# Optimization experiments

Measured on AMD Instinct MI355X. Metric: run time of the kernel, lower is better.

## Reference

```python
import jax, jax.numpy as jnp
import numpy as np

B, T, D_IN, D_OUT, H = 4, 2048, 1024, 1024, 16
HD = D_OUT // H

def setup_inputs() -> dict:
    key = jax.random.key(0)
    ks = jax.random.split(key, 9)
    s_in = 1.0 / np.sqrt(D_IN)
    s_out = 1.0 / np.sqrt(D_OUT)
    return {
        "x": jax.random.normal(ks[0], (B, T, D_IN), jnp.float32),
        "w_q": jax.random.uniform(ks[1], (D_IN, D_OUT), jnp.float32, -s_in, s_in),
        "b_q": jax.random.uniform(ks[2], (D_OUT,), jnp.float32, -s_in, s_in),
        "w_k": jax.random.uniform(ks[3], (D_IN, D_OUT), jnp.float32, -s_in, s_in),
        "b_k": jax.random.uniform(ks[4], (D_OUT,), jnp.float32, -s_in, s_in),
        "w_v": jax.random.uniform(ks[5], (D_IN, D_OUT), jnp.float32, -s_in, s_in),
        "b_v": jax.random.uniform(ks[6], (D_OUT,), jnp.float32, -s_in, s_in),
        "w_o": jax.random.uniform(ks[7], (D_OUT, D_OUT), jnp.float32, -s_out, s_out),
        "b_o": jax.random.uniform(ks[8], (D_OUT,), jnp.float32, -s_out, s_out),
    }

def reference(x, w_q, b_q, w_k, b_k, w_v, b_v, w_o, b_o):
    b, t, _ = x.shape
    # projections -> [b, h, t, hd]
    def split_heads(y):
        return y.reshape(b, t, H, HD).transpose(0, 2, 1, 3)
    q = split_heads(x @ w_q + b_q)
    k = split_heads(x @ w_k + b_k)
    v = split_heads(x @ w_v + b_v)
    scores = jnp.einsum('bhqd,bhkd->bhqk', q, k)
    causal = jnp.triu(jnp.ones((t, t), dtype=bool), k=1)
    scores = jnp.where(causal, -jnp.inf, scores)
    weights = jax.nn.softmax(scores / np.sqrt(HD), axis=-1)
    # dropout_rate = 0.0 -> identity
    ctx = jnp.einsum('bhqk,bhkd->bhqd', weights, v)
    ctx = ctx.transpose(0, 2, 1, 3).reshape(b, t, D_OUT)
    return ctx @ w_o + b_o
```

## Files before the change

### kernel.cpp

```cpp
#include <hip/hip_runtime.h>
#include <hip/hip_bf16.h>
#include <stdint.h>

#define B_N 4
#define T_N 2048
#define D_N 1024
#define H_N 16
#define HD_N 64

typedef __bf16 bf16x8 __attribute__((ext_vector_type(8)));
typedef unsigned short u16x8 __attribute__((ext_vector_type(8)));
typedef unsigned short u16x4 __attribute__((ext_vector_type(4)));
typedef float f32x4 __attribute__((ext_vector_type(4)));
typedef float f32x16 __attribute__((ext_vector_type(16)));

static __device__ __forceinline__ unsigned short f2bf(float f) {
    union { float f; unsigned u; } v; v.f = f;
    unsigned r = v.u + 0x7fffu + ((v.u >> 16) & 1u);
    return (unsigned short)(r >> 16);
}
static __device__ __forceinline__ float bf2f(unsigned short s) {
    union { unsigned u; float f; } v; v.u = ((unsigned)s) << 16;
    return v.f;
}
static __device__ __forceinline__ bf16x8 as_bf(u16x8 v) {
    return __builtin_bit_cast(bf16x8, v);
}
static __device__ __forceinline__ unsigned packbf(float a, float b) {
    union { float f; unsigned u; } x, y; x.f = a; y.f = b;
    return (x.u >> 16) | (y.u & 0xffff0000u);
}
static __device__ __forceinline__ void gload_lds16(const void* g, void* l) {
    __builtin_amdgcn_global_load_lds(
        (const __attribute__((address_space(1))) void*)g,
        (__attribute__((address_space(3))) void*)l, 16, 0, 0);
}

__global__ __launch_bounds__(256) void cvt_x_kernel(const float* __restrict__ x,
                                                    unsigned short* __restrict__ xb) {
    int i = (blockIdx.x * 256 + threadIdx.x) * 8;
    f32x4 a = *(const f32x4*)(x + i);
    f32x4 b = *(const f32x4*)(x + i + 4);
    u16x8 o;
    o[0] = f2bf(a[0]); o[1] = f2bf(a[1]); o[2] = f2bf(a[2]); o[3] = f2bf(a[3]);
    o[4] = f2bf(b[0]); o[5] = f2bf(b[1]); o[6] = f2bf(b[2]); o[7] = f2bf(b[3]);
    *(u16x8*)(xb + i) = o;
}

__global__ __launch_bounds__(256) void cvt_w_t_kernel(
        const float* __restrict__ w0, const float* __restrict__ w1,
        const float* __restrict__ w2, const float* __restrict__ w3,
        unsigned short* __restrict__ o0, unsigned short* __restrict__ o1,
        unsigned short* __restrict__ o2, unsigned short* __restrict__ o3) {
    __shared__ float tile[32][33];
    const float* w; unsigned short* o;
    switch (blockIdx.z) {
        case 0:  w = w0; o = o0; break;
        case 1:  w = w1; o = o1; break;
        case 2:  w = w2; o = o2; break;
        default: w = w3; o = o3; break;
    }
    int n0 = blockIdx.x * 32, k0 = blockIdx.y * 32;
    int tx = threadIdx.x & 31, ty = threadIdx.x >> 5;
    #pragma unroll
    for (int r = 0; r < 4; ++r)
        tile[ty + r * 8][tx] = w[(k0 + ty + r * 8) * 1024 + n0 + tx];
    __syncthreads();
    #pragma unroll
    for (int r = 0; r < 4; ++r)
        o[(n0 + ty + r * 8) * 1024 + k0 + tx] = f2bf(tile[tx][ty + r * 8]);
}

#define BM 128
#define BN 128
#define BK 64

__global__ __launch_bounds__(256) void qkv_gemm_kernel(
        const unsigned short* __restrict__ xb,
        const unsigned short* __restrict__ wt,
        const float* __restrict__ bq, const float* __restrict__ bk,
        const float* __restrict__ bv,
        unsigned short* __restrict__ qws, unsigned short* __restrict__ kws,
        unsigned short* __restrict__ vtws) {
    __shared__ unsigned short As[BM * BK];
    __shared__ unsigned short Bs[BN * BK];
    const int tid = threadIdx.x;
    const int lane = tid & 63, wid = tid >> 6;
    const int wr = wid >> 1, wc = wid & 1;
    const int l15 = lane & 15, lg = lane >> 4;
    const int mbase = blockIdx.y * BM;
    const int nbase = blockIdx.x * BN;

    const int rsub = lane >> 3;
    const int gsw  = (lane & 7) ^ rsub;
    const unsigned short* asrc0 = xb + (mbase + wid * 32 + rsub) * 1024 + gsw * 8;
    const unsigned short* bsrc0 = wt + (nbase + wid * 32 + rsub) * 1024 + gsw * 8;
    char* adst0 = (char*)As + wid * 4096;
    char* bdst0 = (char*)Bs + wid * 4096;

    f32x4 acc[4][4] = {};

    for (int k0 = 0; k0 < 1024; k0 += BK) {
        __syncthreads();
        #pragma unroll
        for (int i = 0; i < 4; ++i)
            gload_lds16(asrc0 + i * 8 * 1024 + k0, adst0 + i * 1024);
        #pragma unroll
        for (int i = 0; i < 4; ++i)
            gload_lds16(bsrc0 + i * 8 * 1024 + k0, bdst0 + i * 1024);
        __syncthreads();
        #pragma unroll
        for (int kk = 0; kk < 2; ++kk) {
            bf16x8 a[4], b[4];
            #pragma unroll
            for (int mi = 0; mi < 4; ++mi) {
                int m = wr * 64 + mi * 16 + l15;
                int g = (kk * 4 + lg) ^ (m & 7);
                a[mi] = as_bf(*(const u16x8*)(As + m * 64 + (g << 3)));
            }
            #pragma unroll
            for (int ni = 0; ni < 4; ++ni) {
                int n = wc * 64 + ni * 16 + l15;
                int g = (kk * 4 + lg) ^ (n & 7);
                b[ni] = as_bf(*(const u16x8*)(Bs + n * 64 + (g << 3)));
            }
            #pragma unroll
            for (int mi = 0; mi < 4; ++mi)
                #pragma unroll
                for (int ni = 0; ni < 4; ++ni)
                    acc[mi][ni] = __builtin_amdgcn_mfma_f32_16x16x32_bf16(
                        a[mi], b[ni], acc[mi][ni], 0, 0, 0);
        }
    }

    const int mat = nbase >> 10;
    const float* bias = (mat == 0) ? bq : (mat == 1) ? bk : bv;
    #pragma unroll
    for (int ni = 0; ni < 4; ++ni) {
        int cg = (nbase & 1023) + wc * 64 + ni * 16 + l15;
        float bb = bias[cg];
        int h = cg >> 6, hd = cg & 63;
        #pragma unroll
        for (int mi = 0; mi < 4; ++mi) {
            int row = mbase + wr * 64 + mi * 16 + lg * 4;
            int bidx = row >> 11;
            int t = row & 2047;
            if (mat == 2) {
                u16x4 pv;
                #pragma unroll
                for (int r = 0; r < 4; ++r) pv[r] = f2bf(acc[mi][ni][r] + bb);
                *(u16x4*)(vtws + ((bidx * 16 + h) * 64 + hd) * 2048 + t) = pv;
            } else {
                unsigned short* dst =
                    ((mat == 0) ? qws : kws) + ((bidx * 16 + h) * 2048 + t) * 64 + hd;
                #pragma unroll
                for (int r = 0; r < 4; ++r) dst[r * 64] = f2bf(acc[mi][ni][r] + bb);
            }
        }
    }
}

#define AQB 128
#define AKV 64

__global__ __launch_bounds__(256, 3) void attn_kernel(
        const unsigned short* __restrict__ qws,
        const unsigned short* __restrict__ kws,
        const unsigned short* __restrict__ vtws,
        unsigned short* __restrict__ ctx) {
    __shared__ unsigned short Ks[2][AKV * 64];
    __shared__ unsigned short Vs[2][64 * AKV];
    __shared__ unsigned short Os[4][32 * 64];

    const int tid = threadIdx.x;
    const int lane = tid & 63, wid = tid >> 6;
    const int l31 = lane & 31, hi = lane >> 5;
    const int qb = 15 - (int)(blockIdx.x >> 6);
    const int bh = blockIdx.x & 63;
    const int qbase = qb * AQB;
    const int qwbase = qbase + wid * 32;
    const unsigned short* qp = qws + bh * 2048 * 64;
    const unsigned short* kp = kws + bh * 2048 * 64;
    const unsigned short* vp = vtws + bh * 64 * 2048;

    const float QSCALE = 0.125f * 1.44269504f;
    bf16x8 qf[4];
    #pragma unroll
    for (int ks = 0; ks < 4; ++ks) {
        u16x8 v = *(const u16x8*)(qp + (qwbase + l31) * 64 + ks * 16 + hi * 8);
        u16x8 o;
        #pragma unroll
        for (int e = 0; e < 8; ++e) o[e] = f2bf(bf2f(v[e]) * QSCALE);
        qf[ks] = as_bf(o);
    }

    f32x16 acc0 = {}, acc1 = {};
    float m_run = -1e30f, lsum = 0.f;

    const int nt = 2 * qb + 2;
    const int wnt = 2 * qb + 1 + (wid >> 1);

    u16x8 kr[2], vr[2];
    #pragma unroll
    for (int it = 0; it < 2; ++it) {
        int flat = it * 256 + tid, r = flat >> 3, g = flat & 7;
        kr[it] = *(const u16x8*)(kp + r * 64 + g * 8);
        vr[it] = *(const u16x8*)(vp + r * 2048 + g * 8);
    }
    #pragma unroll
    for (int it = 0; it < 2; ++it) {
        int flat = it * 256 + tid, r = flat >> 3, g = flat & 7;
        *(u16x8*)(&Ks[0][r * 64 + ((g ^ (r & 7)) << 3)]) = kr[it];
        *(u16x8*)(&Vs[0][r * 64 + ((g ^ (r & 7)) << 3)]) = vr[it];
    }
    __syncthreads();

    for (int t = 0; t < nt; ++t) {
        const int cur = t & 1;
        const int kt = t * AKV;
        if (t + 1 < nt) {
            int kt2 = kt + AKV;
            #pragma unroll
            for (int it = 0; it < 2; ++it) {
                int flat = it * 256 + tid, r = flat >> 3, g = flat & 7;
                kr[it] = *(const u16x8*)(kp + (kt2 + r) * 64 + g * 8);
                vr[it] = *(const u16x8*)(vp + r * 2048 + kt2 + g * 8);
            }
        }
        if (t < wnt) {
            const unsigned short* kb = &Ks[cur][0];
            const unsigned short* vb = &Vs[cur][0];
            #pragma unroll
            for (int half = 0; half < 2; ++half) {
                const int kvbase = kt + half * 32;
                if (kvbase > qwbase + 31) continue;
                f32x16 st = {};
                #pragma unroll
                for (int ks = 0; ks < 4; ++ks) {
                    int row = half * 32 + l31;
                    int g = (ks * 2 + hi) ^ (row & 7);
                    bf16x8 kf = as_bf(*(const u16x8*)(kb + row * 64 + (g << 3)));
                    st = __builtin_amdgcn_mfma_f32_32x32x16_bf16(kf, qf[ks], st, 0, 0, 0);
                }
                if (kvbase + 31 > qwbase) {
                    int q = qwbase + l31;
                    #pragma unroll
                    for (int r = 0; r < 16; ++r) {
                        int kv = kvbase + (r & 3) + 8 * (r >> 2) + 4 * hi;
                        if (kv > q) st[r] = -1e30f;
                    }
                }
                float pmax = st[0];
                #pragma unroll
                for (int r = 1; r < 16; ++r) pmax = fmaxf(pmax, st[r]);
                pmax = fmaxf(pmax, __shfl_xor(pmax, 32));
                if (!__all(pmax - m_run <= 11.5f)) {
                    float mnew = fmaxf(m_run, pmax);
                    float alpha = __builtin_amdgcn_exp2f(m_run - mnew);
                    m_run = mnew;
                    lsum *= alpha;
                    #pragma unroll
                    for (int r = 0; r < 16; ++r) { acc0[r] *= alpha; acc1[r] *= alpha; }
                }
                float p[16];
                float ls = 0.f;
                #pragma unroll
                for (int r = 0; r < 16; ++r) {
                    p[r] = __builtin_amdgcn_exp2f(st[r] - m_run);
                    ls += p[r];
                }
                lsum += ls;
                unsigned c[8], x[8];
                #pragma unroll
                for (int i = 0; i < 8; ++i) c[i] = packbf(p[2 * i], p[2 * i + 1]);
                #pragma unroll
                for (int i = 0; i < 8; ++i) x[i] = (unsigned)__shfl_xor((int)c[i], 32);
                union { u16x8 v; unsigned w[4]; } pb0, pb1;
                pb0.w[0] = hi ? x[2] : c[0];
                pb0.w[1] = hi ? x[3] : c[1];
                pb0.w[2] = hi ? c[2] : x[0];
                pb0.w[3] = hi ? c[3] : x[1];
                pb1.w[0] = hi ? x[6] : c[4];
                pb1.w[1] = hi ? x[7] : c[5];
                pb1.w[2] = hi ? c[6] : x[4];
                pb1.w[3] = hi ? c[7] : x[5];
                #pragma unroll
                for (int db = 0; db < 2; ++db) {
                    f32x16& accd = db ? acc1 : acc0;
                    #pragma unroll
                    for (int ks2 = 0; ks2 < 2; ++ks2) {
                        int row = db * 32 + l31;
                        int g = (half * 4 + ks2 * 2 + hi) ^ (row & 7);
                        bf16x8 vf = as_bf(*(const u16x8*)(vb + row * 64 + (g << 3)));
                        accd = __builtin_amdgcn_mfma_f32_32x32x16_bf16(
                            vf, ks2 ? pb1.v : pb0.v, accd, 0, 0, 0);
                    }
                }
            }
        }
        __syncthreads();
        if (t + 1 < nt) {
            unsigned short* dk = &Ks[cur ^ 1][0];
            unsigned short* dv = &Vs[cur ^ 1][0];
            #pragma unroll
            for (int it = 0; it < 2; ++it) {
                int flat = it * 256 + tid, r = flat >> 3, g = flat & 7;
                *(u16x8*)(dk + r * 64 + ((g ^ (r & 7)) << 3)) = kr[it];
                *(u16x8*)(dv + r * 64 + ((g ^ (r & 7)) << 3)) = vr[it];
            }
        }
        __syncthreads();
    }

    lsum += __shfl_xor(lsum, 32);
    float rinv = __builtin_amdgcn_rcpf(lsum);
    unsigned short* ow = &Os[wid][0];
    #pragma unroll
    for (int db = 0; db < 2; ++db) {
        const f32x16& accd = db ? acc1 : acc0;
        #pragma unroll
        for (int r = 0; r < 16; r += 2) {
            int d = db * 32 + (r & 3) + 8 * (r >> 2) + 4 * hi;
            unsigned w = packbf(accd[r] * rinv, accd[r + 1] * rinv);
            int g = (d >> 3) ^ (l31 & 7);
            *(unsigned*)(ow + l31 * 64 + (g << 3) + (d & 7)) = w;
        }
    }
    __syncthreads();
    const int bidx = bh >> 4, h = bh & 15;
    #pragma unroll
    for (int rr = 0; rr < 4; ++rr) {
        int flat = rr * 64 + lane;
        int q = flat >> 3, g = flat & 7;
        u16x8 v = *(const u16x8*)(ow + q * 64 + ((g ^ (q & 7)) << 3));
        int qg = qbase + wid * 32 + q;
        *(u16x8*)(ctx + (bidx * 2048 + qg) * 1024 + h * 64 + g * 8) = v;
    }
}

__global__ __launch_bounds__(256) void out_gemm_kernel(
        const unsigned short* __restrict__ ctx,
        const unsigned short* __restrict__ wot,
        const float* __restrict__ bo,
        float* __restrict__ out) {
    __shared__ unsigned short As[BM * BK];
    __shared__ unsigned short Bs[BN * BK];
    const int tid = threadIdx.x;
    const int lane = tid & 63, wid = tid >> 6;
    const int wr = wid >> 1, wc = wid & 1;
    const int l15 = lane & 15, lg = lane >> 4;
    const int mbase = blockIdx.y * BM;
    const int nbase = blockIdx.x * BN;

    const int rsub = lane >> 3;
    const int gsw  = (lane & 7) ^ rsub;
    const unsigned short* asrc0 = ctx + (mbase + wid * 32 + rsub) * 1024 + gsw * 8;
    const unsigned short* bsrc0 = wot + (nbase + wid * 32 + rsub) * 1024 + gsw * 8;
    char* adst0 = (char*)As + wid * 4096;
    char* bdst0 = (char*)Bs + wid * 4096;

    f32x4 acc[4][4] = {};

    for (int k0 = 0; k0 < 1024; k0 += BK) {
        __syncthreads();
        #pragma unroll
        for (int i = 0; i < 4; ++i)
            gload_lds16(asrc0 + i * 8 * 1024 + k0, adst0 + i * 1024);
        #pragma unroll
        for (int i = 0; i < 4; ++i)
            gload_lds16(bsrc0 + i * 8 * 1024 + k0, bdst0 + i * 1024);
        __syncthreads();
        #pragma unroll
        for (int kk = 0; kk < 2; ++kk) {
            bf16x8 a[4], b[4];
            #pragma unroll
            for (int mi = 0; mi < 4; ++mi) {
                int m = wr * 64 + mi * 16 + l15;
                int g = (kk * 4 + lg) ^ (m & 7);
                a[mi] = as_bf(*(const u16x8*)(As + m * 64 + (g << 3)));
            }
            #pragma unroll
            for (int ni = 0; ni < 4; ++ni) {
                int n = wc * 64 + ni * 16 + l15;
                int g = (kk * 4 + lg) ^ (n & 7);
                b[ni] = as_bf(*(const u16x8*)(Bs + n * 64 + (g << 3)));
            }
            #pragma unroll
            for (int mi = 0; mi < 4; ++mi)
                #pragma unroll
                for (int ni = 0; ni < 4; ++ni)
                    acc[mi][ni] = __builtin_amdgcn_mfma_f32_16x16x32_bf16(
                        a[mi], b[ni], acc[mi][ni], 0, 0, 0);
        }
    }

    #pragma unroll
    for (int ni = 0; ni < 4; ++ni) {
        int ncol = nbase + wc * 64 + ni * 16 + l15;
        float bb = bo[ncol];
        #pragma unroll
        for (int mi = 0; mi < 4; ++mi) {
            int row = mbase + wr * 64 + mi * 16 + lg * 4;
            #pragma unroll
            for (int r = 0; r < 4; ++r)
                out[(row + r) * 1024 + ncol] = acc[mi][ni][r] + bb;
        }
    }
}

extern "C" void kernel_launch(void* const* d_in, const int* in_sizes, int n_in,
                              void* d_out, int out_size, void* d_ws, size_t ws_size,
                              hipStream_t stream) {
    const float* x  = (const float*)d_in[0];
    const float* wq = (const float*)d_in[1];
    const float* bq = (const float*)d_in[2];
    const float* wk = (const float*)d_in[3];
    const float* bk = (const float*)d_in[4];
    const float* wv = (const float*)d_in[5];
    const float* bv = (const float*)d_in[6];
    const float* wo = (const float*)d_in[7];
    const float* bo = (const float*)d_in[8];
    float* out = (float*)d_out;

    char* ws = (char*)d_ws;
    unsigned short* xb   = (unsigned short*)(ws);
    unsigned short* wqt  = (unsigned short*)(ws + (16u << 20));
    unsigned short* wkt  = (unsigned short*)(ws + (18u << 20));
    unsigned short* wvt  = (unsigned short*)(ws + (20u << 20));
    unsigned short* wot  = (unsigned short*)(ws + (22u << 20));
    unsigned short* qws  = (unsigned short*)(ws + (24u << 20));
    unsigned short* kws  = (unsigned short*)(ws + (40u << 20));
    unsigned short* vtws = (unsigned short*)(ws + (56u << 20));
    unsigned short* ctx  = (unsigned short*)(ws + (72u << 20));

    cvt_x_kernel<<<4096, 256, 0, stream>>>(x, xb);
    cvt_w_t_kernel<<<dim3(32, 32, 4), 256, 0, stream>>>(wq, wk, wv, wo,
                                                        wqt, wkt, wvt, wot);
    qkv_gemm_kernel<<<dim3(24, 64), 256, 0, stream>>>(xb, wqt, bq, bk, bv,
                                                      qws, kws, vtws);
    attn_kernel<<<1024, 256, 0, stream>>>(qws, kws, vtws, ctx);
    out_gemm_kernel<<<dim3(8, 64), 256, 0, stream>>>(ctx, wot, bo, out);
}
```

Measured before the change: 250.1 us.

## Double-buffer LDS in projection GEMMs and remap blocks across XCDs

Both projection GEMMs now keep two LDS buffers and prefetch the k-tile two steps ahead with direct global-to-LDS loads. Explicit vmcnt waits, barriers and setprio around the MFMA bursts let memory traffic overlap with compute instead of stalling on a full sync every k-step. The launch becomes a 1D grid whose block index is remapped so that consecutive tiles land on the same XCD, which should improve L2 reuse of shared A and B panels. This doubles LDS use per block, which may lower occupancy, and the hand-written waitcnt counts must match the number of loads in flight.

```diff
diff --git a/kernel.cpp b/kernel.cpp
--- a/kernel.cpp
+++ b/kernel.cpp
@@ -71,9 +71,7 @@
         o[(n0 + ty + r * 8) * 1024 + k0 + tx] = f2bf(tile[tx][ty + r * 8]);
 }
 
-#define BM 128
-#define BN 128
-#define BK 64
+#define GNT 16
 
 __global__ __launch_bounds__(256) void qkv_gemm_kernel(
         const unsigned short* __restrict__ xb,
@@ -82,54 +80,101 @@
         const float* __restrict__ bv,
         unsigned short* __restrict__ qws, unsigned short* __restrict__ kws,
         unsigned short* __restrict__ vtws) {
-    __shared__ unsigned short As[BM * BK];
-    __shared__ unsigned short Bs[BN * BK];
+    __shared__ unsigned short As[2][128 * 64];
+    __shared__ unsigned short Bs[2][128 * 64];
     const int tid = threadIdx.x;
     const int lane = tid & 63, wid = tid >> 6;
     const int wr = wid >> 1, wc = wid & 1;
     const int l15 = lane & 15, lg = lane >> 4;
-    const int mbase = blockIdx.y * BM;
-    const int nbase = blockIdx.x * BN;
-
+    const int cpx = (int)gridDim.x >> 3;
+    const int s = ((int)blockIdx.x & 7) * cpx + ((int)blockIdx.x >> 3);
+    const int by = s / 24, bx = s - by * 24;
+    const int mbase = by * 128, nbase = bx * 128;
     const int rsub = lane >> 3;
     const int gsw  = (lane & 7) ^ rsub;
-    const unsigned short* asrc0 = xb + (mbase + wid * 32 + rsub) * 1024 + gsw * 8;
-    const unsigned short* bsrc0 = wt + (nbase + wid * 32 + rsub) * 1024 + gsw * 8;
-    char* adst0 = (char*)As + wid * 4096;
-    char* bdst0 = (char*)Bs + wid * 4096;
+    const unsigned short* ags = xb + (mbase + wid * 8 + rsub) * 1024 + gsw * 8;
+    const unsigned short* bgs = wt + (nbase + wid * 8 + rsub) * 1024 + gsw * 8;
+    const int dstE = wid * 8 * 64;
 
     f32x4 acc[4][4] = {};
 
-    for (int k0 = 0; k0 < 1024; k0 += BK) {
-        __syncthreads();
+    auto STAGE = [&](int T, int BUF) {
+        const unsigned short* a_ = ags + T * 64;
+        const unsigned short* b_ = bgs + T * 64;
         #pragma unroll
         for (int i = 0; i < 4; ++i)
-            gload_lds16(asrc0 + i * 8 * 1024 + k0, adst0 + i * 1024);
+            gload_lds16(a_ + i * 32 * 1024, (void*)&As[BUF][dstE + i * 32 * 64]);
         #pragma unroll
         for (int i = 0; i < 4; ++i)
-            gload_lds16(bsrc0 + i * 8 * 1024 + k0, bdst0 + i * 1024);
-        __syncthreads();
-        #pragma unroll
-        for (int kk = 0; kk < 2; ++kk) {
-            bf16x8 a[4], b[4];
+            gload_lds16(b_ + i * 32 * 1024, (void*)&Bs[BUF][dstE + i * 32 * 64]);
+    };
+
+    STAGE(0, 0);
+    STAGE(1, 1);
+    asm volatile("s_waitcnt vmcnt(8)" ::: "memory");
+    __builtin_amdgcn_s_barrier();
+    asm volatile("" ::: "memory");
+
+    for (int t = 0; t < GNT; ++t) {
+        const int b = t & 1;
+        const unsigned short* Ab = &As[b][0];
+        const unsigned short* Bb = &Bs[b][0];
+        {
+            bf16x8 af[4], bfr[4];
             #pragma unroll
             for (int mi = 0; mi < 4; ++mi) {
                 int m = wr * 64 + mi * 16 + l15;
-                int g = (kk * 4 + lg) ^ (m & 7);
-                a[mi] = as_bf(*(const u16x8*)(As + m * 64 + (g << 3)));
+                int g = lg ^ (m & 7);
+                af[mi] = as_bf(*(const u16x8*)(Ab + m * 64 + (g << 3)));
             }
             #pragma unroll
             for (int ni = 0; ni < 4; ++ni) {
                 int n = wc * 64 + ni * 16 + l15;
-                int g = (kk * 4 + lg) ^ (n & 7);
-                b[ni] = as_bf(*(const u16x8*)(Bs + n * 64 + (g << 3)));
-            }
+                int g = lg ^ (n & 7);
+                bfr[ni] = as_bf(*(const u16x8*)(Bb + n * 64 + (g << 3)));
+            }
+            __builtin_amdgcn_s_barrier();
+            __builtin_amdgcn_s_setprio(1);
             #pragma unroll
             for (int mi = 0; mi < 4; ++mi)
                 #pragma unroll
                 for (int ni = 0; ni < 4; ++ni)
                     acc[mi][ni] = __builtin_amdgcn_mfma_f32_16x16x32_bf16(
-                        a[mi], b[ni], acc[mi][ni], 0, 0, 0);
+                        af[mi], bfr[ni], acc[mi][ni], 0, 0, 0);
+            __builtin_amdgcn_s_setprio(0);
+            __builtin_amdgcn_s_barrier();
+            asm volatile("" ::: "memory");
+        }
+        {
+            bf16x8 af[4], bfr[4];
+            #pragma unroll
+            for (int mi = 0; mi < 4; ++mi) {
+                int m = wr * 64 + mi * 16 + l15;
+                int g = (4 + lg) ^ (m & 7);
+                af[mi] = as_bf(*(const u16x8*)(Ab + m * 64 + (g << 3)));
+            }
+            #pragma unroll
+            for (int ni = 0; ni < 4; ++ni) {
+                int n = wc * 64 + ni * 16 + l15;
+                int g = (4 + lg) ^ (n & 7);
+                bfr[ni] = as_bf(*(const u16x8*)(Bb + n * 64 + (g << 3)));
+            }
+            asm volatile("s_waitcnt lgkmcnt(0)" ::: "memory");
+            __builtin_amdgcn_s_barrier();
+            asm volatile("" ::: "memory");
+            if (t + 2 < GNT) STAGE(t + 2, b);
+            __builtin_amdgcn_s_setprio(1);
+            #pragma unroll
+            for (int mi = 0; mi < 4; ++mi)
+                #pragma unroll
+                for (int ni = 0; ni < 4; ++ni)
+                    acc[mi][ni] = __builtin_amdgcn_mfma_f32_16x16x32_bf16(
+                        af[mi], bfr[ni], acc[mi][ni], 0, 0, 0);
+            __builtin_amdgcn_s_setprio(0);
+            if (t + 2 < GNT)      { asm volatile("s_waitcnt vmcnt(8)" ::: "memory"); }
+            else if (t + 1 < GNT) { asm volatile("s_waitcnt vmcnt(0)" ::: "memory"); }
+            __builtin_amdgcn_s_barrier();
+            asm volatile("" ::: "memory");
         }
     }
 
@@ -343,54 +388,101 @@
         const unsigned short* __restrict__ wot,
         const float* __restrict__ bo,
         float* __restrict__ out) {
-    __shared__ unsigned short As[BM * BK];
-    __shared__ unsigned short Bs[BN * BK];
+    __shared__ unsigned short As[2][128 * 64];
+    __shared__ unsigned short Bs[2][128 * 64];
     const int tid = threadIdx.x;
     const int lane = tid & 63, wid = tid >> 6;
     const int wr = wid >> 1, wc = wid & 1;
     const int l15 = lane & 15, lg = lane >> 4;
-    const int mbase = blockIdx.y * BM;
-    const int nbase = blockIdx.x * BN;
-
+    const int cpx = (int)gridDim.x >> 3;
+    const int s = ((int)blockIdx.x & 7) * cpx + ((int)blockIdx.x >> 3);
+    const int by = s >> 3, bx = s & 7;
+    const int mbase = by * 128, nbase = bx * 128;
     const int rsub = lane >> 3;
     const int gsw  = (lane & 7) ^ rsub;
-    const unsigned short* asrc0 = ctx + (mbase + wid * 32 + rsub) * 1024 + gsw * 8;
-    const unsigned short* bsrc0 = wot + (nbase + wid * 32 + rsub) * 1024 + gsw * 8;
-    char* adst0 = (char*)As + wid * 4096;
-    char* bdst0 = (char*)Bs + wid * 4096;
+    const unsigned short* ags = ctx + (mbase + wid * 8 + rsub) * 1024 + gsw * 8;
+    const unsigned short* bgs = wot + (nbase + wid * 8 + rsub) * 1024 + gsw * 8;
+    const int dstE = wid * 8 * 64;
 
     f32x4 acc[4][4] = {};
 
-    for (int k0 = 0; k0 < 1024; k0 += BK) {
-        __syncthreads();
+    auto STAGE = [&](int T, int BUF) {
+        const unsigned short* a_ = ags + T * 64;
+        const unsigned short* b_ = bgs + T * 64;
         #pragma unroll
         for (int i = 0; i < 4; ++i)
-            gload_lds16(asrc0 + i * 8 * 1024 + k0, adst0 + i * 1024);
+            gload_lds16(a_ + i * 32 * 1024, (void*)&As[BUF][dstE + i * 32 * 64]);
         #pragma unroll
         for (int i = 0; i < 4; ++i)
-            gload_lds16(bsrc0 + i * 8 * 1024 + k0, bdst0 + i * 1024);
-        __syncthreads();
-        #pragma unroll
-        for (int kk = 0; kk < 2; ++kk) {
-            bf16x8 a[4], b[4];
+            gload_lds16(b_ + i * 32 * 1024, (void*)&Bs[BUF][dstE + i * 32 * 64]);
+    };
+
+    STAGE(0, 0);
+    STAGE(1, 1);
+    asm volatile("s_waitcnt vmcnt(8)" ::: "memory");
+    __builtin_amdgcn_s_barrier();
+    asm volatile("" ::: "memory");
+
+    for (int t = 0; t < GNT; ++t) {
+        const int b = t & 1;
+        const unsigned short* Ab = &As[b][0];
+        const unsigned short* Bb = &Bs[b][0];
+        {
+            bf16x8 af[4], bfr[4];
             #pragma unroll
             for (int mi = 0; mi < 4; ++mi) {
                 int m = wr * 64 + mi * 16 + l15;
-                int g = (kk * 4 + lg) ^ (m & 7);
-                a[mi] = as_bf(*(const u16x8*)(As + m * 64 + (g << 3)));
+                int g = lg ^ (m & 7);
+                af[mi] = as_bf(*(const u16x8*)(Ab + m * 64 + (g << 3)));
             }
             #pragma unroll
             for (int ni = 0; ni < 4; ++ni) {
                 int n = wc * 64 + ni * 16 + l15;
-                int g = (kk * 4 + lg) ^ (n & 7);
-                b[ni] = as_bf(*(const u16x8*)(Bs + n * 64 + (g << 3)));
-            }
+                int g = lg ^ (n & 7);
+                bfr[ni] = as_bf(*(const u16x8*)(Bb + n * 64 + (g << 3)));
+            }
+            __builtin_amdgcn_s_barrier();
+            __builtin_amdgcn_s_setprio(1);
             #pragma unroll
             for (int mi = 0; mi < 4; ++mi)
                 #pragma unroll
                 for (int ni = 0; ni < 4; ++ni)
                     acc[mi][ni] = __builtin_amdgcn_mfma_f32_16x16x32_bf16(
-                        a[mi], b[ni], acc[mi][ni], 0, 0, 0);
+                        af[mi], bfr[ni], acc[mi][ni], 0, 0, 0);
+            __builtin_amdgcn_s_setprio(0);
+            __builtin_amdgcn_s_barrier();
+            asm volatile("" ::: "memory");
+        }
+        {
+            bf16x8 af[4], bfr[4];
+            #pragma unroll
+            for (int mi = 0; mi < 4; ++mi) {
+                int m = wr * 64 + mi * 16 + l15;
+                int g = (4 + lg) ^ (m & 7);
+                af[mi] = as_bf(*(const u16x8*)(Ab + m * 64 + (g << 3)));
+            }
+            #pragma unroll
+            for (int ni = 0; ni < 4; ++ni) {
+                int n = wc * 64 + ni * 16 + l15;
+                int g = (4 + lg) ^ (n & 7);
+                bfr[ni] = as_bf(*(const u16x8*)(Bb + n * 64 + (g << 3)));
+            }
+            asm volatile("s_waitcnt lgkmcnt(0)" ::: "memory");
+            __builtin_amdgcn_s_barrier();
+            asm volatile("" ::: "memory");
+            if (t + 2 < GNT) STAGE(t + 2, b);
+            __builtin_amdgcn_s_setprio(1);
+            #pragma unroll
+            for (int mi = 0; mi < 4; ++mi)
+                #pragma unroll
+                for (int ni = 0; ni < 4; ++ni)
+                    acc[mi][ni] = __builtin_amdgcn_mfma_f32_16x16x32_bf16(
+                        af[mi], bfr[ni], acc[mi][ni], 0, 0, 0);
+            __builtin_amdgcn_s_setprio(0);
+            if (t + 2 < GNT)      { asm volatile("s_waitcnt vmcnt(8)" ::: "memory"); }
+            else if (t + 1 < GNT) { asm volatile("s_waitcnt vmcnt(0)" ::: "memory"); }
+            __builtin_amdgcn_s_barrier();
+            asm volatile("" ::: "memory");
         }
     }
 
@@ -436,8 +528,8 @@
     cvt_x_kernel<<<4096, 256, 0, stream>>>(x, xb);
     cvt_w_t_kernel<<<dim3(32, 32, 4), 256, 0, stream>>>(wq, wk, wv, wo,
                                                         wqt, wkt, wvt, wot);
-    qkv_gemm_kernel<<<dim3(24, 64), 256, 0, stream>>>(xb, wqt, bq, bk, bv,
-                                                      qws, kws, vtws);
+    qkv_gemm_kernel<<<1536, 256, 0, stream>>>(xb, wqt, bq, bk, bv,
+                                              qws, kws, vtws);
     attn_kernel<<<1024, 256, 0, stream>>>(qws, kws, vtws, ctx);
-    out_gemm_kernel<<<dim3(8, 64), 256, 0, stream>>>(ctx, wot, bo, out);
-}
+    out_gemm_kernel<<<512, 256, 0, stream>>>(ctx, wot, bo, out);
+}
```

New measurement: 253.8 us. Within noise of the previous version (+1.5%).
